# Performance work log

Measured on AMD Instinct MI355X. Metric: run time of the kernel, lower is better.

The kernel has to match this reference:

```python
import jax, jax.numpy as jnp
import numpy as np

B, T, C = 4, 2048, 1024
H = 16  # NUM_HEADS
HD = C // H  # head_dim = 64


def setup_inputs() -> dict:
    key = jax.random.key(0)
    k1, k2, k3 = jax.random.split(key, 3)
    x = jax.random.normal(k1, (B, T, C), dtype=jnp.float32)
    # nn.Linear weights: stored as [out, in]; apply as x @ W.T
    W_attn = jax.random.normal(k2, (3 * C, C), dtype=jnp.float32) * (1.0 / np.sqrt(C))
    W_proj = jax.random.normal(k3, (C, C), dtype=jnp.float32) * (1.0 / np.sqrt(C))
    return {"x": x, "W_attn": W_attn, "W_proj": W_proj}


def reference(x, W_attn, W_proj):
    Bv, Tv, Cv = x.shape
    qkv = x @ W_attn.T  # [B, T, 3C]
    q, k, v = jnp.split(qkv, 3, axis=2)
    # [B, H, T, HD]
    q = q.reshape(Bv, Tv, H, HD).transpose(0, 2, 1, 3)
    k = k.reshape(Bv, Tv, H, HD).transpose(0, 2, 1, 3)
    v = v.reshape(Bv, Tv, H, HD).transpose(0, 2, 1, 3)
    att = jnp.einsum("bhqd,bhkd->bhqk", q, k) * (1.0 / np.sqrt(HD))
    causal = jnp.tril(jnp.ones((Tv, Tv), dtype=bool))
    att = jnp.where(causal[None, None, :, :], att, -jnp.inf)
    att = jax.nn.softmax(att, axis=-1)
    y = jnp.einsum("bhqk,bhkd->bhqd", att, v)
    y = y.transpose(0, 2, 1, 3).reshape(Bv, Tv, Cv)
    return y @ W_proj.T
```

## Files before the change

### kernel.cpp

```cpp
#include <hip/hip_runtime.h>

typedef _Float16 f16;
typedef _Float16 half8 __attribute__((ext_vector_type(8)));
typedef _Float16 half4v __attribute__((ext_vector_type(4)));
typedef __fp16 fp16x2 __attribute__((ext_vector_type(2)));
typedef float floatx4 __attribute__((ext_vector_type(4)));
typedef unsigned int uint;

constexpr int Bsz = 4, Tseq = 2048, Cdim = 1024, NH = 16, HDim = 64;
constexpr int Mtok = Bsz * Tseq;
constexpr int NQT = Tseq / 64;
constexpr float QSCALE = 0.18033688f;

#define GLDS16(src, dst) __builtin_amdgcn_global_load_lds( \
    (const __attribute__((address_space(1))) void*)(src),  \
    (__attribute__((address_space(3))) void*)(dst), 16, 0, 0)

__device__ __forceinline__ float fexp2(float x) { return __builtin_amdgcn_exp2f(x); }
__device__ __forceinline__ uint pkrtz(float a, float b) {
  fp16x2 h = __builtin_amdgcn_cvt_pkrtz(a, b);
  return __builtin_bit_cast(uint, h);
}

__global__ void cvt3_kernel(const float* __restrict__ x, const float* __restrict__ wa,
                            const float* __restrict__ wp,
                            f16* __restrict__ xh, f16* __restrict__ wah, f16* __restrict__ wph) {
  constexpr int nx = Mtok * Cdim, nwa = 3 * Cdim * Cdim, nwp = Cdim * Cdim;
  int i = (blockIdx.x * blockDim.x + threadIdx.x) * 4;
  const float* src; f16* dst; int off;
  if (i < nx)            { src = x;  dst = xh;  off = i; }
  else if (i < nx + nwa) { src = wa; dst = wah; off = i - nx; }
  else                   { src = wp; dst = wph; off = i - nx - nwa; }
  float4 v = *(const float4*)(src + off);
  half4v o;
  o[0] = (f16)v.x; o[1] = (f16)v.y; o[2] = (f16)v.z; o[3] = (f16)v.w;
  *(half4v*)(dst + off) = o;
}

template<int EPI>
__device__ __forceinline__ void gemm_body(f16* As, f16* Bs,
    const f16* __restrict__ X, const f16* __restrict__ W,
    float* __restrict__ outF,
    f16* __restrict__ q_out, f16* __restrict__ k_out, f16* __restrict__ v_out,
    int N, int K, int bm, int bn)
{
  constexpr int BK = 32;
  const int tid = threadIdx.x;
  const int wave = tid >> 6;
  const int lane = tid & 63;
  const int g = lane >> 4, lm = lane & 15;
  const int m0 = bm * 128, n0 = bn * 128;
  const int wr = wave >> 1, wc = wave & 1;

  floatx4 acc[4][4];
#pragma unroll
  for (int i = 0; i < 4; ++i)
#pragma unroll
    for (int j = 0; j < 4; ++j) acc[i][j] = (floatx4)0.0f;

  for (int k0 = 0; k0 < K; k0 += BK) {
    __syncthreads();
#pragma unroll
    for (int t = 0; t < 2; ++t) {
      int row = (wave * 2 + t) * 16 + (lane >> 2);
      int cg = (lane & 3) ^ ((row >> 1) & 3);
      GLDS16(X + (size_t)(m0 + row) * K + k0 + cg * 8,
             (char*)As + (wave * 2 + t) * 1024);
      GLDS16(W + (size_t)(n0 + row) * K + k0 + cg * 8,
             (char*)Bs + (wave * 2 + t) * 1024);
    }
    __syncthreads();

    half8 af[4], bf[4];
#pragma unroll
    for (int i = 0; i < 4; ++i) {
      int rowa = wr * 64 + i * 16 + lm;
      int cga = g ^ ((rowa >> 1) & 3);
      af[i] = *(const half8*)((const char*)As + rowa * 64 + cga * 16);
      int rowb = wc * 64 + i * 16 + lm;
      int cgb = g ^ ((rowb >> 1) & 3);
      bf[i] = *(const half8*)((const char*)Bs + rowb * 64 + cgb * 16);
    }
#pragma unroll
    for (int i = 0; i < 4; ++i)
#pragma unroll
      for (int j = 0; j < 4; ++j)
        acc[i][j] = __builtin_amdgcn_mfma_f32_16x16x32_f16(af[i], bf[j], acc[i][j], 0, 0, 0);
  }

#pragma unroll
  for (int i = 0; i < 4; ++i) {
#pragma unroll
    for (int j = 0; j < 4; ++j) {
#pragma unroll
      for (int r = 0; r < 4; ++r) {
        int m = m0 + wr * 64 + i * 16 + 4 * g + r;
        int n = n0 + wc * 64 + j * 16 + lm;
        float v = acc[i][j][r];
        if constexpr (EPI == 1) {
          outF[(size_t)m * N + n] = v;
        } else if constexpr (EPI == 0) {
          int which = n >> 10;
          int inner = n & 1023;
          int h = inner >> 6, hd = inner & 63;
          int b = m >> 11, t = m & 2047;
          if (which == 0) {
            v *= QSCALE;
            q_out[(((size_t)(b * NH + h)) * Tseq + t) * HDim + hd] = (f16)v;
          } else {
            k_out[(((size_t)(b * NH + h)) * Tseq + t) * HDim + hd] = (f16)v;
          }
        } else {
          int h = m >> 6, hd = m & 63;
          int b = n >> 11, t = n & 2047;
          v_out[(((size_t)(b * NH + h)) * HDim + hd) * Tseq + t] = (f16)v;
        }
      }
    }
  }
}

__global__ __launch_bounds__(256)
void qkv_kernel(const f16* __restrict__ xh, const f16* __restrict__ wAh,
                f16* __restrict__ Qh, f16* __restrict__ Kh, f16* __restrict__ Vth) {
  __shared__ __align__(16) f16 As[128 * 32];
  __shared__ __align__(16) f16 Bs[128 * 32];
  const int x = blockIdx.x & 7;
  const int q = blockIdx.x >> 3;
  if (q < 128) {
    int c = q >> 4, u = q & 15;
    int bm = x * 8 + (c >> 2) * 4 + (u >> 2);
    int bn = (c & 3) * 4 + (u & 3);
    gemm_body<0>(As, Bs, xh, wAh, nullptr, Qh, Kh, nullptr, 2048, Cdim, bm, bn);
  } else {
    int v = q - 128;
    gemm_body<2>(As, Bs, wAh + (size_t)2048 * Cdim, xh, nullptr, nullptr, nullptr, Vth,
                 Mtok, Cdim, x, v);
  }
}

__global__ __launch_bounds__(256)
void proj_kernel(const f16* __restrict__ yh, const f16* __restrict__ wPh, float* __restrict__ out) {
  __shared__ __align__(16) f16 As[128 * 32];
  __shared__ __align__(16) f16 Bs[128 * 32];
  const int x = blockIdx.x & 7;
  const int u = blockIdx.x >> 3;
  int c = u >> 4, w = u & 15;
  int bm = x * 8 + (c >> 1) * 4 + (w >> 2);
  int bn = (c & 1) * 4 + (w & 3);
  gemm_body<1>(As, Bs, yh, wPh, out, nullptr, nullptr, nullptr, Cdim, Cdim, bm, bn);
}

__device__ __forceinline__ void softmax_tile(floatx4* s, float& l_run,
                                             bool diag, int j0, int qg, char* pwrow, int g, int lm) {
  if (diag) {
#pragma unroll
    for (int nf = 0; nf < 4; ++nf)
#pragma unroll
      for (int r = 0; r < 4; ++r)
        if (j0 + nf * 16 + 4 * g + r > qg) s[nf][r] = -1e30f;
  }
  float rs = 0.f;
#pragma unroll
  for (int nf = 0; nf < 4; ++nf) {
    float p0 = fexp2(s[nf][0]), p1 = fexp2(s[nf][1]);
    float p2 = fexp2(s[nf][2]), p3 = fexp2(s[nf][3]);
    rs += (p0 + p1) + (p2 + p3);
    uint lo = pkrtz(p0, p1), hi = pkrtz(p2, p3);
    int slot = 2 * nf + (g >> 1);
    uint2 u; u.x = lo; u.y = hi;
    *(uint2*)(pwrow + 16 * (slot ^ (lm & 7)) + 8 * (g & 1)) = u;
  }
  l_run += rs;
}

__device__ __forceinline__ void store_o(const floatx4* acc, float l, int q0w, int g, int lm,
                                        f16* __restrict__ Y, int b, int h) {
  l += __shfl_xor(l, 16, 64);
  l += __shfl_xor(l, 32, 64);
#pragma unroll
  for (int r = 0; r < 4; ++r) {
    float lq = __shfl(l, 4 * g + r, 64);
    float inv = 1.0f / lq;
    int t = q0w + 4 * g + r;
    size_t base = ((size_t)(b * Tseq + t)) * Cdim + h * HDim;
#pragma unroll
    for (int ng = 0; ng < 4; ++ng)
      Y[base + ng * 16 + lm] = (f16)(acc[ng][r] * inv);
  }
}

__global__ __launch_bounds__(256)
void attn_kernel(const f16* __restrict__ Q, const f16* __restrict__ Kg,
                 const f16* __restrict__ Vt, f16* __restrict__ Y)
{
  __shared__ __align__(16) char smem[40960];
  int wg = blockIdx.x;
  int lin = (wg & 7) * 128 + (wg >> 3);
  const int p  = lin & 15;
  const int bh = lin >> 4;
  const int itB = NQT - p;
  const f16* Qb  = Q  + (size_t)bh * Tseq * HDim;
  const f16* Kb  = Kg + (size_t)bh * Tseq * HDim;
  const f16* Vtb = Vt + (size_t)bh * HDim * Tseq;

  const int tid = threadIdx.x, w = tid >> 6, lane = tid & 63;
  const int g = lane >> 4, lm = lane & 15;
  char* pwrow = smem + 32768 + w * 2048 + lm * 128;
  const int b = bh >> 4, h = bh & 15;

  int q0 = (NQT - 1 - p) * 64;
  int qg = q0 + w * 16 + lm;
  half8 qf0 = *(const half8*)(Qb + (size_t)(q0 + w * 16 + lm) * HDim + g * 8);
  half8 qf1 = *(const half8*)(Qb + (size_t)(q0 + w * 16 + lm) * HDim + 32 + g * 8);

  floatx4 acc[4];
  float l = 0.f;
#pragma unroll
  for (int ng = 0; ng < 4; ++ng) acc[ng] = (floatx4)0.f;

  const int srow = w * 8 + (lane >> 3);
  const int sslot = lane & 7;

  auto stage = [&](int j0s, int buf) {
#pragma unroll
    for (int t = 0; t < 2; ++t) {
      int row = srow + t * 32;
      int cg = sslot ^ (row & 7);
      GLDS16(Kb + (size_t)(j0s + row) * HDim + cg * 8,
             smem + buf * 8192 + (w * 8 + t * 32) * 128);
      GLDS16(Vtb + (size_t)row * Tseq + j0s + cg * 8,
             smem + 16384 + buf * 8192 + (w * 8 + t * 32) * 128);
    }
  };

  stage(0, 0);
  asm volatile("s_waitcnt vmcnt(0)" ::: "memory");
  __builtin_amdgcn_s_barrier();

  for (int it = 0; it < NQT + 1; ++it) {
    const bool lastB = (it == itB - 1);
    const bool last  = (it == NQT);
    const int jt = (it < itB) ? it : it - itB;
    const int j0 = jt * 64;

    if (!last) {
      const int itn = it + 1;
      const int jtn = (itn < itB) ? itn : itn - itB;
      stage(jtn * 64, itn & 1);
    }

    char* kb   = smem + (it & 1) * 8192;
    char* vbuf = smem + 16384 + (it & 1) * 8192;

    floatx4 s[4];
    __builtin_amdgcn_s_setprio(1);
#pragma unroll
    for (int nf = 0; nf < 4; ++nf) {
      half8 kf0 = *(const half8*)(kb + (nf * 16 + lm) * 128 + 16 * ((g)     ^ (lm & 7)));
      half8 kf1 = *(const half8*)(kb + (nf * 16 + lm) * 128 + 16 * ((4 + g) ^ (lm & 7)));
      s[nf] = __builtin_amdgcn_mfma_f32_16x16x32_f16(kf0, qf0, (floatx4)0.f, 0, 0, 0);
      s[nf] = __builtin_amdgcn_mfma_f32_16x16x32_f16(kf1, qf1, s[nf], 0, 0, 0);
    }
    __builtin_amdgcn_s_setprio(0);

    softmax_tile(s, l, lastB || last, j0, qg, pwrow, g, lm);
    half8 pa0 = *(const half8*)(pwrow + 16 * ((g)     ^ (lm & 7)));
    half8 pa1 = *(const half8*)(pwrow + 16 * ((4 + g) ^ (lm & 7)));

    __builtin_amdgcn_s_setprio(1);
#pragma unroll
    for (int c = 0; c < 2; ++c)
#pragma unroll
      for (int ng = 0; ng < 4; ++ng) {
        half8 vbf = *(const half8*)(vbuf + (ng * 16 + lm) * 128 + 16 * ((4 * c + g) ^ (lm & 7)));
        acc[ng] = __builtin_amdgcn_mfma_f32_16x16x32_f16(c ? pa1 : pa0, vbf, acc[ng], 0, 0, 0);
      }
    __builtin_amdgcn_s_setprio(0);

    asm volatile("s_waitcnt vmcnt(0)" ::: "memory");
    __builtin_amdgcn_s_barrier();

    if (lastB) {
      store_o(acc, l, q0 + 16 * w, g, lm, Y, b, h);
      q0 = p * 64;
      qg = q0 + w * 16 + lm;
      qf0 = *(const half8*)(Qb + (size_t)(q0 + w * 16 + lm) * HDim + g * 8);
      qf1 = *(const half8*)(Qb + (size_t)(q0 + w * 16 + lm) * HDim + 32 + g * 8);
      l = 0.f;
#pragma unroll
      for (int ng = 0; ng < 4; ++ng) acc[ng] = (floatx4)0.f;
    }
  }

  store_o(acc, l, q0 + 16 * w, g, lm, Y, b, h);
}

extern "C" void kernel_launch(void* const* d_in, const int* in_sizes, int n_in,
                              void* d_out, int out_size, void* d_ws, size_t ws_size,
                              hipStream_t stream)
{
  const float* x      = (const float*)d_in[0];
  const float* W_attn = (const float*)d_in[1];
  const float* W_proj = (const float*)d_in[2];
  float* out = (float*)d_out;

  char* ws = (char*)d_ws;
  f16* xh  = (f16*)(ws);
  f16* wAh = (f16*)(ws + (size_t)(16u << 20));
  f16* wPh = (f16*)(ws + (size_t)(22u << 20));
  f16* Qh  = (f16*)(ws + (size_t)(24u << 20));
  f16* Kh  = (f16*)(ws + (size_t)(40u << 20));
  f16* Vth = (f16*)(ws + (size_t)(56u << 20));
  f16* yh  = xh;

  constexpr int ntot = (Mtok * Cdim + 3 * Cdim * Cdim + Cdim * Cdim) / 4;
  cvt3_kernel<<<(ntot + 255) / 256, 256, 0, stream>>>(x, W_attn, W_proj, xh, wAh, wPh);

  qkv_kernel<<<dim3(1536), 256, 0, stream>>>(xh, wAh, Qh, Kh, Vth);

  attn_kernel<<<dim3(1024), 256, 0, stream>>>(Qh, Kh, Vth, yh);

  proj_kernel<<<dim3(512), 256, 0, stream>>>(yh, wPh, out);
}
```

Baseline: 172.3 us.

## Split QKV GEMM into large-tile pipelined QK kernel and separate V kernel

The Q/K part of the QKV projection moves to a new kernel with 256x256 tiles, 512 threads, BK=64, and double-buffered direct-to-LDS loads. Loads for the next K-step are interleaved with four MFMA phases, using explicit waitcnt, barriers and priority hints. The transposed V projection becomes its own launch on the old 128x128 gemm body. This aims to raise data reuse and overlap memory with MFMA work, at the cost of an extra launch, 128KB of LDS per block, and fewer blocks (256) in the QK grid.

```diff
diff --git a/kernel.cpp b/kernel.cpp
--- a/kernel.cpp
+++ b/kernel.cpp
@@ -21,6 +21,7 @@
   fp16x2 h = __builtin_amdgcn_cvt_pkrtz(a, b);
   return __builtin_bit_cast(uint, h);
 }
+#define MFMA16(a, b, c) __builtin_amdgcn_mfma_f32_16x16x32_f16((a), (b), (c), 0, 0, 0)
 
 __global__ void cvt3_kernel(const float* __restrict__ x, const float* __restrict__ wa,
                             const float* __restrict__ wp,
@@ -37,11 +38,160 @@
   *(half4v*)(dst + off) = o;
 }
 
+__global__ __launch_bounds__(512, 2)
+void qk8p_kernel(const f16* __restrict__ X, const f16* __restrict__ W,
+                 f16* __restrict__ q_out, f16* __restrict__ k_out)
+{
+  __shared__ __align__(16) char smem[131072];
+  constexpr int K = 1024, NT = 16;
+  const int sbid = (blockIdx.x & 7) * 32 + (blockIdx.x >> 3);
+  const int bm = sbid >> 3, bn = sbid & 7;
+  const int m0 = bm * 256, n0 = bn * 256;
+  const int tid = threadIdx.x, w = tid >> 6, lane = tid & 63;
+  const int wr = w >> 2, wc = w & 3;
+  const int g = lane >> 4, lm = lane & 15;
+
+  const int grow = lane >> 3;
+  const int cg = (lane & 7) ^ grow;
+
+  auto stage_half = [&](int op, int t, int h) {
+    const f16* src = op ? W : X;
+    char* base = smem + op * 65536 + (t & 1) * 32768 + h * 16384;
+    const int rbase = (op ? n0 : m0) + h * 128;
+#pragma unroll
+    for (int r2 = 0; r2 < 2; ++r2) {
+      int row = rbase + r2 * 64 + w * 8 + grow;
+      GLDS16(src + (size_t)row * K + t * 64 + cg * 8,
+             base + (r2 * 64 + w * 8) * 128);
+    }
+  };
+
+  floatx4 acc[8][4];
+#pragma unroll
+  for (int i = 0; i < 8; ++i)
+#pragma unroll
+    for (int j = 0; j < 4; ++j) acc[i][j] = (floatx4)0.0f;
+
+  const int sw = lm & 7;
+  const char* S = smem;
+  const int Abase = wr * 16384 + lm * 128;
+  const int Bbase = 65536 + (wc >> 1) * 16384 + ((wc & 1) * 64 + lm) * 128;
+
+  half8 a0[4][2], a1[4][2], b0[2][2], b1[2][2];
+
+  stage_half(0, 0, 0); stage_half(0, 0, 1);
+  stage_half(1, 0, 0); stage_half(1, 0, 1);
+  stage_half(1, 1, 0); stage_half(1, 1, 1);
+
+#pragma unroll 2
+  for (int t = 0; t < NT; ++t) {
+    const int par = (t & 1) * 32768;
+
+    if (t == NT - 1) { asm volatile("s_waitcnt vmcnt(0)" ::: "memory"); }
+    else             { asm volatile("s_waitcnt vmcnt(4)" ::: "memory"); }
+    __builtin_amdgcn_s_barrier();
+#pragma unroll
+    for (int i = 0; i < 4; ++i)
+#pragma unroll
+      for (int kk = 0; kk < 2; ++kk)
+        a0[i][kk] = *(const half8*)(S + par + Abase + i * 2048 + 16 * ((kk * 4 + g) ^ sw));
+#pragma unroll
+    for (int j = 0; j < 2; ++j)
+#pragma unroll
+      for (int kk = 0; kk < 2; ++kk)
+        b0[j][kk] = *(const half8*)(S + par + Bbase + j * 2048 + 16 * ((kk * 4 + g) ^ sw));
+    if (t + 1 < NT) stage_half(0, t + 1, 0);
+    asm volatile("s_waitcnt lgkmcnt(0)" ::: "memory");
+    __builtin_amdgcn_sched_barrier(0);
+    __builtin_amdgcn_s_setprio(1);
+#pragma unroll
+    for (int i = 0; i < 4; ++i)
+#pragma unroll
+      for (int j = 0; j < 2; ++j)
+#pragma unroll
+        for (int kk = 0; kk < 2; ++kk)
+          acc[i][j] = MFMA16(a0[i][kk], b0[j][kk], acc[i][j]);
+    __builtin_amdgcn_s_setprio(0);
+
+    __builtin_amdgcn_s_barrier();
+#pragma unroll
+    for (int j = 0; j < 2; ++j)
+#pragma unroll
+      for (int kk = 0; kk < 2; ++kk)
+        b1[j][kk] = *(const half8*)(S + par + Bbase + (j + 2) * 2048 + 16 * ((kk * 4 + g) ^ sw));
+    if (t + 1 < NT) stage_half(0, t + 1, 1);
+    asm volatile("s_waitcnt lgkmcnt(0)" ::: "memory");
+    __builtin_amdgcn_sched_barrier(0);
+    __builtin_amdgcn_s_setprio(1);
+#pragma unroll
+    for (int i = 0; i < 4; ++i)
+#pragma unroll
+      for (int j = 0; j < 2; ++j)
+#pragma unroll
+        for (int kk = 0; kk < 2; ++kk)
+          acc[i][j + 2] = MFMA16(a0[i][kk], b1[j][kk], acc[i][j + 2]);
+    __builtin_amdgcn_s_setprio(0);
+
+    __builtin_amdgcn_s_barrier();
+#pragma unroll
+    for (int i = 0; i < 4; ++i)
+#pragma unroll
+      for (int kk = 0; kk < 2; ++kk)
+        a1[i][kk] = *(const half8*)(S + par + Abase + (i + 4) * 2048 + 16 * ((kk * 4 + g) ^ sw));
+    if (t + 2 < NT) stage_half(1, t + 2, 0);
+    asm volatile("s_waitcnt lgkmcnt(0)" ::: "memory");
+    __builtin_amdgcn_sched_barrier(0);
+    __builtin_amdgcn_s_setprio(1);
+#pragma unroll
+    for (int i = 0; i < 4; ++i)
+#pragma unroll
+      for (int j = 0; j < 2; ++j)
+#pragma unroll
+        for (int kk = 0; kk < 2; ++kk)
+          acc[i + 4][j + 2] = MFMA16(a1[i][kk], b1[j][kk], acc[i + 4][j + 2]);
+    __builtin_amdgcn_s_setprio(0);
+
+    __builtin_amdgcn_s_barrier();
+    if (t + 2 < NT) stage_half(1, t + 2, 1);
+    __builtin_amdgcn_s_setprio(1);
+#pragma unroll
+    for (int i = 0; i < 4; ++i)
+#pragma unroll
+      for (int j = 0; j < 2; ++j)
+#pragma unroll
+        for (int kk = 0; kk < 2; ++kk)
+          acc[i + 4][j] = MFMA16(a1[i][kk], b0[j][kk], acc[i + 4][j]);
+    __builtin_amdgcn_s_setprio(0);
+  }
+
+#pragma unroll
+  for (int i = 0; i < 8; ++i) {
+#pragma unroll
+    for (int j = 0; j < 4; ++j) {
+#pragma unroll
+      for (int r = 0; r < 4; ++r) {
+        int m = m0 + wr * 128 + i * 16 + 4 * g + r;
+        int n = n0 + wc * 64 + j * 16 + lm;
+        float v = acc[i][j][r];
+        int which = n >> 10;
+        int inner = n & 1023;
+        int h = inner >> 6, hd = inner & 63;
+        int b = m >> 11, t = m & 2047;
+        if (which == 0) {
+          v *= QSCALE;
+          q_out[(((size_t)(b * NH + h)) * Tseq + t) * HDim + hd] = (f16)v;
+        } else {
+          k_out[(((size_t)(b * NH + h)) * Tseq + t) * HDim + hd] = (f16)v;
+        }
+      }
+    }
+  }
+}
+
 template<int EPI>
 __device__ __forceinline__ void gemm_body(f16* As, f16* Bs,
     const f16* __restrict__ X, const f16* __restrict__ W,
-    float* __restrict__ outF,
-    f16* __restrict__ q_out, f16* __restrict__ k_out, f16* __restrict__ v_out,
+    float* __restrict__ outF, f16* __restrict__ v_out,
     int N, int K, int bm, int bn)
 {
   constexpr int BK = 32;
@@ -85,7 +235,7 @@
     for (int i = 0; i < 4; ++i)
 #pragma unroll
       for (int j = 0; j < 4; ++j)
-        acc[i][j] = __builtin_amdgcn_mfma_f32_16x16x32_f16(af[i], bf[j], acc[i][j], 0, 0, 0);
+        acc[i][j] = MFMA16(af[i], bf[j], acc[i][j]);
   }
 
 #pragma unroll
@@ -99,17 +249,6 @@
         float v = acc[i][j][r];
         if constexpr (EPI == 1) {
           outF[(size_t)m * N + n] = v;
-        } else if constexpr (EPI == 0) {
-          int which = n >> 10;
-          int inner = n & 1023;
-          int h = inner >> 6, hd = inner & 63;
-          int b = m >> 11, t = m & 2047;
-          if (which == 0) {
-            v *= QSCALE;
-            q_out[(((size_t)(b * NH + h)) * Tseq + t) * HDim + hd] = (f16)v;
-          } else {
-            k_out[(((size_t)(b * NH + h)) * Tseq + t) * HDim + hd] = (f16)v;
-          }
         } else {
           int h = m >> 6, hd = m & 63;
           int b = n >> 11, t = n & 2047;
@@ -121,22 +260,11 @@
 }
 
 __global__ __launch_bounds__(256)
-void qkv_kernel(const f16* __restrict__ xh, const f16* __restrict__ wAh,
-                f16* __restrict__ Qh, f16* __restrict__ Kh, f16* __restrict__ Vth) {
+void vt_kernel(const f16* __restrict__ xh, const f16* __restrict__ wVh, f16* __restrict__ Vth) {
   __shared__ __align__(16) f16 As[128 * 32];
   __shared__ __align__(16) f16 Bs[128 * 32];
-  const int x = blockIdx.x & 7;
-  const int q = blockIdx.x >> 3;
-  if (q < 128) {
-    int c = q >> 4, u = q & 15;
-    int bm = x * 8 + (c >> 2) * 4 + (u >> 2);
-    int bn = (c & 3) * 4 + (u & 3);
-    gemm_body<0>(As, Bs, xh, wAh, nullptr, Qh, Kh, nullptr, 2048, Cdim, bm, bn);
-  } else {
-    int v = q - 128;
-    gemm_body<2>(As, Bs, wAh + (size_t)2048 * Cdim, xh, nullptr, nullptr, nullptr, Vth,
-                 Mtok, Cdim, x, v);
-  }
+  int bm = blockIdx.x & 7, bn = blockIdx.x >> 3;
+  gemm_body<2>(As, Bs, wVh, xh, nullptr, Vth, Mtok, Cdim, bm, bn);
 }
 
 __global__ __launch_bounds__(256)
@@ -145,10 +273,10 @@
   __shared__ __align__(16) f16 Bs[128 * 32];
   const int x = blockIdx.x & 7;
   const int u = blockIdx.x >> 3;
-  int c = u >> 4, w = u & 15;
-  int bm = x * 8 + (c >> 1) * 4 + (w >> 2);
-  int bn = (c & 1) * 4 + (w & 3);
-  gemm_body<1>(As, Bs, yh, wPh, out, nullptr, nullptr, nullptr, Cdim, Cdim, bm, bn);
+  int c = u >> 4, ww = u & 15;
+  int bm = x * 8 + (c >> 1) * 4 + (ww >> 2);
+  int bn = (c & 1) * 4 + (ww & 3);
+  gemm_body<1>(As, Bs, yh, wPh, out, nullptr, Cdim, Cdim, bm, bn);
 }
 
 __device__ __forceinline__ void softmax_tile(floatx4* s, float& l_run,
@@ -259,8 +387,8 @@
     for (int nf = 0; nf < 4; ++nf) {
       half8 kf0 = *(const half8*)(kb + (nf * 16 + lm) * 128 + 16 * ((g)     ^ (lm & 7)));
       half8 kf1 = *(const half8*)(kb + (nf * 16 + lm) * 128 + 16 * ((4 + g) ^ (lm & 7)));
-      s[nf] = __builtin_amdgcn_mfma_f32_16x16x32_f16(kf0, qf0, (floatx4)0.f, 0, 0, 0);
-      s[nf] = __builtin_amdgcn_mfma_f32_16x16x32_f16(kf1, qf1, s[nf], 0, 0, 0);
+      s[nf] = MFMA16(kf0, qf0, (floatx4)0.f);
+      s[nf] = MFMA16(kf1, qf1, s[nf]);
     }
     __builtin_amdgcn_s_setprio(0);
 
@@ -274,7 +402,7 @@
 #pragma unroll
       for (int ng = 0; ng < 4; ++ng) {
         half8 vbf = *(const half8*)(vbuf + (ng * 16 + lm) * 128 + 16 * ((4 * c + g) ^ (lm & 7)));
-        acc[ng] = __builtin_amdgcn_mfma_f32_16x16x32_f16(c ? pa1 : pa0, vbf, acc[ng], 0, 0, 0);
+        acc[ng] = MFMA16(c ? pa1 : pa0, vbf, acc[ng]);
       }
     __builtin_amdgcn_s_setprio(0);
 
@@ -317,7 +445,9 @@
   constexpr int ntot = (Mtok * Cdim + 3 * Cdim * Cdim + Cdim * Cdim) / 4;
   cvt3_kernel<<<(ntot + 255) / 256, 256, 0, stream>>>(x, W_attn, W_proj, xh, wAh, wPh);
 
-  qkv_kernel<<<dim3(1536), 256, 0, stream>>>(xh, wAh, Qh, Kh, Vth);
+  qk8p_kernel<<<dim3(256), 512, 0, stream>>>(xh, wAh, Qh, Kh);
+
+  vt_kernel<<<dim3(512), 256, 0, stream>>>(xh, wAh + (size_t)2048 * Cdim, Vth);
 
   attn_kernel<<<dim3(1024), 256, 0, stream>>>(Qh, Kh, Vth, yh);
 
```

Measured after the change: 168.6 us. -2.1%, faster.
